# Kernel optimization log

Measured on AMD Instinct MI355X. Metric: run time of the kernel, lower is better.

Reference implementation:

```python
import jax, jax.numpy as jnp
import numpy as np

HIDDEN = 1024
NUM_HEADS = 16
HEAD_DIM = HIDDEN // NUM_HEADS
LN_EPS = 1e-12


def setup_inputs() -> dict:
    key = jax.random.key(0)
    ks = jax.random.split(key, 12)
    B, S, H = 4, 2048, HIDDEN
    scale = 0.02
    return {
        "hidden_states": jax.random.normal(ks[0], (B, S, H), dtype=jnp.float32),
        "attention_mask": jnp.zeros((B, 1, 1, S), dtype=jnp.float32),
        "Wq": jax.random.normal(ks[1], (H, H), dtype=jnp.float32) * scale,
        "bq": jnp.zeros((H,), dtype=jnp.float32),
        "Wk": jax.random.normal(ks[2], (H, H), dtype=jnp.float32) * scale,
        "bk": jnp.zeros((H,), dtype=jnp.float32),
        "Wv": jax.random.normal(ks[3], (H, H), dtype=jnp.float32) * scale,
        "bv": jnp.zeros((H,), dtype=jnp.float32),
        "Wo": jax.random.normal(ks[4], (H, H), dtype=jnp.float32) * scale,
        "bo": jnp.zeros((H,), dtype=jnp.float32),
        "ln_gamma": jnp.ones((H,), dtype=jnp.float32),
        "ln_beta": jnp.zeros((H,), dtype=jnp.float32),
    }


def _split_heads(x):  # [B,S,H] -> [B,nh,S,hd]
    B, S, _ = x.shape
    return x.reshape(B, S, NUM_HEADS, HEAD_DIM).transpose(0, 2, 1, 3)


def reference(hidden_states, attention_mask, Wq, bq, Wk, bk, Wv, bv, Wo, bo, ln_gamma, ln_beta):
    # QKV projections (torch Linear: x @ W.T + b)
    q = _split_heads(hidden_states @ Wq.T + bq)
    k = _split_heads(hidden_states @ Wk.T + bk)
    v = _split_heads(hidden_states @ Wv.T + bv)
    # scaled dot-product attention with additive mask (dropout=identity, eval)
    scores = jnp.einsum('bhqd,bhkd->bhqk', q, k) / jnp.sqrt(jnp.float32(HEAD_DIM))
    scores = scores + attention_mask
    probs = jax.nn.softmax(scores, axis=-1)
    ctx = jnp.einsum('bhqk,bhkd->bhqd', probs, v)
    B, _, S, _ = ctx.shape
    ctx = ctx.transpose(0, 2, 1, 3).reshape(B, S, HIDDEN)
    # output projection + residual + LayerNorm
    out = ctx @ Wo.T + bo + hidden_states
    mu = jnp.mean(out, axis=-1, keepdims=True)
    var = jnp.mean(jnp.square(out - mu), axis=-1, keepdims=True)
    return (out - mu) * jax.lax.rsqrt(var + LN_EPS) * ln_gamma + ln_beta
```

## Files before the change

### kernel.cpp

```cpp
#include <hip/hip_runtime.h>
#include <stdint.h>

#define SEQ   2048
#define BATCH 4
#define NH    16
#define HD    64
#define H     1024
#define QKVN  3072

typedef unsigned short u16;
typedef unsigned int   u32;
typedef __bf16 bf16x8 __attribute__((ext_vector_type(8)));
typedef float  f32x4  __attribute__((ext_vector_type(4)));
typedef unsigned int v2u  __attribute__((ext_vector_type(2)));
typedef unsigned int u32x4 __attribute__((ext_vector_type(4)));

#define MFMA16(a, b, c) __builtin_amdgcn_mfma_f32_16x16x32_bf16((a), (b), (c), 0, 0, 0)
#define LOG2E 1.4426950408889634f

__device__ __forceinline__ u16 f2bf(float f) {
  u32 u = __float_as_uint(f);
  u = (u + 0x7fffu + ((u >> 16) & 1u)) >> 16;
  return (u16)u;
}

__device__ __forceinline__ void gload16(const u16* g, u16* l) {
  __builtin_amdgcn_global_load_lds(
      (const __attribute__((address_space(1))) u32*)g,
      (__attribute__((address_space(3))) u32*)l, 16, 0, 0);
}

__device__ __forceinline__ u32 lds_addr(const void* p) {
  return (u32)(uintptr_t)(const __attribute__((address_space(3))) void*)p;
}

__global__ __launch_bounds__(256) void cast_all(
    const float* __restrict__ hid, const float* __restrict__ wq,
    const float* __restrict__ wk,  const float* __restrict__ wv,
    const float* __restrict__ wo,
    u16* __restrict__ hb, u16* __restrict__ wqkv, u16* __restrict__ wo_b)
{
  int i = blockIdx.x * 256 + threadIdx.x;
  const float* s; u16* d; int idx;
  if (i < 2097152) { s = hid; d = hb; idx = i; }
  else {
    int j = i - 2097152;
    int w = j >> 18; idx = j & 262143;
    if      (w == 0) { s = wq; d = wqkv; }
    else if (w == 1) { s = wk; d = wqkv + 1048576; }
    else if (w == 2) { s = wv; d = wqkv + 2097152; }
    else             { s = wo; d = wo_b; }
  }
  float4 v = ((const float4*)s)[idx];
  ushort4 o;
  o.x = f2bf(v.x); o.y = f2bf(v.y); o.z = f2bf(v.z); o.w = f2bf(v.w);
  ((ushort4*)d)[idx] = o;
}

template<int EPI>
__global__ __launch_bounds__(256, 2) void gemm_bf16(
    const u16* __restrict__ A, const u16* __restrict__ B,
    u16* __restrict__ outb, float* __restrict__ outf, int ldc,
    const float* __restrict__ b0, const float* __restrict__ b1,
    const float* __restrict__ b2, const float* __restrict__ resid)
{
  __shared__ __align__(16) u16 As[128 * 32];
  __shared__ __align__(16) u16 Bs[128 * 32];
  const int tid = threadIdx.x;
  const int lane = tid & 63;
  const int wv = tid >> 6, wr = wv >> 1, wc = wv & 1;
  const int l15 = lane & 15, l4 = lane >> 4;

  const int nwg = gridDim.x * gridDim.y;
  const int flat = blockIdx.y * gridDim.x + blockIdx.x;
  const int swz = (flat & 7) * (nwg >> 3) + (flat >> 3);
  const int row0 = (swz / gridDim.x) * 128, col0 = (swz % gridDim.x) * 128;

  const f32x4 fz = {0.f, 0.f, 0.f, 0.f};
  f32x4 acc[4][4];
#pragma unroll
  for (int i = 0; i < 4; ++i)
#pragma unroll
    for (int j = 0; j < 4; ++j) acc[i][j] = fz;

  const int srow = lane >> 2;
  const int skol = (lane & 3) * 8;
  const u16* Ab = A + (size_t)(row0 + srow) * 1024 + skol;
  const u16* Bb = B + (size_t)(col0 + srow) * 1024 + skol;
  const int c0 = wv * 2;

  for (int kt = 0; kt < 1024; kt += 32) {
    gload16(Ab + (size_t)(c0 * 16) * 1024 + kt,       &As[(c0 * 16) * 32]);
    gload16(Ab + (size_t)(c0 * 16 + 16) * 1024 + kt,  &As[(c0 * 16 + 16) * 32]);
    gload16(Bb + (size_t)(c0 * 16) * 1024 + kt,       &Bs[(c0 * 16) * 32]);
    gload16(Bb + (size_t)(c0 * 16 + 16) * 1024 + kt,  &Bs[(c0 * 16 + 16) * 32]);
    __syncthreads();

    bf16x8 af[4], bfr[4];
#pragma unroll
    for (int f = 0; f < 4; ++f) {
      af[f]  = *(const bf16x8*)&As[(wr * 64 + f * 16 + l15) * 32 + l4 * 8];
      bfr[f] = *(const bf16x8*)&Bs[(wc * 64 + f * 16 + l15) * 32 + l4 * 8];
    }
#pragma unroll
    for (int i = 0; i < 4; ++i)
#pragma unroll
      for (int j = 0; j < 4; ++j)
        acc[i][j] = MFMA16(af[i], bfr[j], acc[i][j]);
    __syncthreads();
  }

  if (EPI == 0) {
    const float* bias = (col0 < 1024) ? b0 : (col0 < 2048) ? b1 : b2;
#pragma unroll
    for (int i = 0; i < 4; ++i) {
      int gr0 = row0 + wr * 64 + i * 16 + l4 * 4;
#pragma unroll
      for (int j = 0; j < 4; ++j) {
        int gc = col0 + wc * 64 + j * 16 + l15;
        float bv = bias[gc & 1023];
#pragma unroll
        for (int r = 0; r < 4; ++r)
          outb[(size_t)(gr0 + r) * ldc + gc] = f2bf(acc[i][j][r] + bv);
      }
    }
  } else {
#pragma unroll
    for (int i = 0; i < 4; ++i) {
      int gr0 = row0 + wr * 64 + i * 16 + l4 * 4;
#pragma unroll
      for (int j = 0; j < 4; ++j) {
        int gc = col0 + wc * 64 + j * 16 + l15;
        float bv = b0[gc];
#pragma unroll
        for (int r = 0; r < 4; ++r) {
          size_t idx = (size_t)(gr0 + r) * ldc + gc;
          outf[idx] = acc[i][j][r] + bv + resid[idx];
        }
      }
    }
  }
}

__global__ __launch_bounds__(256, 2) void flash_attn(
    const u16* __restrict__ qkv, const float* __restrict__ mask,
    u16* __restrict__ ctxb)
{
  __shared__ __align__(16) u16 PQs[128 * 72];
  __shared__ __align__(16) u16 Ks[64 * 72];
  __shared__ __align__(16) u16 Vs[4096];

  const int flat = (blockIdx.z * 16 + blockIdx.y) * 16 + blockIdx.x;
  const int swzb = (flat & 7) * 128 + (flat >> 3);
  const int qt = swzb & 15, h = (swzb >> 4) & 15, b = swzb >> 8;

  const int tid = threadIdx.x, lane = tid & 63, wv = tid >> 6;
  const int l15 = lane & 15, l4 = lane >> 4;

  const size_t tokb = (size_t)b * SEQ;
  const u16* Qg = qkv + (tokb + (size_t)qt * 128) * QKVN + h * HD;
  const u16* Kg = qkv + tokb * QKVN + 1024 + h * HD;
  const u16* Vg = qkv + tokb * QKVN + 2048 + h * HD;
  const float* maskp = mask + (size_t)b * SEQ;

#pragma unroll
  for (int cc = 0; cc < 4; ++cc) {
    int c = tid + cc * 256;
    int r = c >> 3, ko = (c & 7) * 8;
    *(uint4*)&PQs[r * 72 + ko] = *(const uint4*)&Qg[(size_t)r * QKVN + ko];
  }
  __syncthreads();
  bf16x8 qf[2][2];
#pragma unroll
  for (int qfi = 0; qfi < 2; ++qfi)
#pragma unroll
    for (int ka = 0; ka < 2; ++ka)
      qf[qfi][ka] = *(const bf16x8*)&PQs[(wv * 32 + qfi * 16 + l15) * 72 + ka * 32 + l4 * 8];

  const f32x4 fz = {0.f, 0.f, 0.f, 0.f};
  float m_run[2][4], l_run[2][4];
  f32x4 ctx[2][4];
#pragma unroll
  for (int qfi = 0; qfi < 2; ++qfi)
#pragma unroll
    for (int r = 0; r < 4; ++r) { m_run[qfi][r] = -1e30f; l_run[qfi][r] = 0.f; }
#pragma unroll
  for (int qfi = 0; qfi < 2; ++qfi)
#pragma unroll
    for (int d = 0; d < 4; ++d) ctx[qfi][d] = fz;

  const int sr = tid >> 3, sk = (tid & 7) * 8;
  const int vso = (sk >> 4) * 1024 + (sk & 15);
  const u32 vaddr0 = lds_addr(&Vs[0]) + lane * 8 + (lane >> 4) * 128;

  uint4 kr0, kr1, vr0, vr1;
  kr0 = *(const uint4*)&Kg[(size_t)sr * QKVN + sk];
  kr1 = *(const uint4*)&Kg[(size_t)(sr + 32) * QKVN + sk];
  vr0 = *(const uint4*)&Vg[(size_t)sr * QKVN + sk];
  vr1 = *(const uint4*)&Vg[(size_t)(sr + 32) * QKVN + sk];

  for (int kv0 = 0; kv0 < SEQ; kv0 += 64) {
    *(uint4*)&Ks[sr * 72 + sk]        = kr0;
    *(uint4*)&Ks[(sr + 32) * 72 + sk] = kr1;
    *(uint4*)&Vs[vso + sr * 16]        = vr0;
    *(uint4*)&Vs[vso + (sr + 32) * 16] = vr1;
    __syncthreads();

    if (kv0 + 64 < SEQ) {
      kr0 = *(const uint4*)&Kg[(size_t)(kv0 + 64 + sr) * QKVN + sk];
      kr1 = *(const uint4*)&Kg[(size_t)(kv0 + 96 + sr) * QKVN + sk];
      vr0 = *(const uint4*)&Vg[(size_t)(kv0 + 64 + sr) * QKVN + sk];
      vr1 = *(const uint4*)&Vg[(size_t)(kv0 + 96 + sr) * QKVN + sk];
    }

    f32x4 s[2][4];
    __builtin_amdgcn_s_setprio(1);
#pragma unroll
    for (int nch = 0; nch < 4; ++nch) {
      bf16x8 kf0 = *(const bf16x8*)&Ks[(nch * 16 + l15) * 72 + l4 * 8];
      bf16x8 kf1 = *(const bf16x8*)&Ks[(nch * 16 + l15) * 72 + 32 + l4 * 8];
#pragma unroll
      for (int qfi = 0; qfi < 2; ++qfi) {
        f32x4 a = fz;
        a = MFMA16(qf[qfi][0], kf0, a);
        a = MFMA16(qf[qfi][1], kf1, a);
        s[qfi][nch] = a;
      }
    }
    __builtin_amdgcn_s_setprio(0);
    float mv[4];
#pragma unroll
    for (int nch = 0; nch < 4; ++nch) mv[nch] = maskp[kv0 + nch * 16 + l15] * LOG2E;
#pragma unroll
    for (int qfi = 0; qfi < 2; ++qfi)
#pragma unroll
      for (int nch = 0; nch < 4; ++nch)
#pragma unroll
        for (int r = 0; r < 4; ++r)
          s[qfi][nch][r] = s[qfi][nch][r] * (0.125f * LOG2E) + mv[nch];

#pragma unroll
    for (int qfi = 0; qfi < 2; ++qfi) {
      float mx[4], rs[4];
#pragma unroll
      for (int r = 0; r < 4; ++r)
        mx[r] = fmaxf(fmaxf(s[qfi][0][r], s[qfi][1][r]), fmaxf(s[qfi][2][r], s[qfi][3][r]));
#pragma unroll
      for (int d = 1; d < 16; d <<= 1)
#pragma unroll
        for (int r = 0; r < 4; ++r) mx[r] = fmaxf(mx[r], __shfl_xor(mx[r], d));
      bool need = false;
#pragma unroll
      for (int r = 0; r < 4; ++r) need |= (mx[r] > m_run[qfi][r] + 11.5415603f);
      if (__any((int)need)) {
#pragma unroll
        for (int r = 0; r < 4; ++r) {
          float mn = fmaxf(m_run[qfi][r], mx[r]);
          float al = exp2f(m_run[qfi][r] - mn);
          m_run[qfi][r] = mn;
          l_run[qfi][r] *= al;
#pragma unroll
          for (int d = 0; d < 4; ++d) ctx[qfi][d][r] *= al;
        }
      }
#pragma unroll
      for (int r = 0; r < 4; ++r) rs[r] = 0.f;
#pragma unroll
      for (int nch = 0; nch < 4; ++nch)
#pragma unroll
        for (int r = 0; r < 4; ++r) {
          float p = exp2f(s[qfi][nch][r] - m_run[qfi][r]);
          rs[r] += p;
          PQs[(wv * 32 + qfi * 16 + l4 * 4 + r) * 72 + nch * 16 + l15] = f2bf(p);
        }
#pragma unroll
      for (int d = 1; d < 16; d <<= 1)
#pragma unroll
        for (int r = 0; r < 4; ++r) rs[r] += __shfl_xor(rs[r], d);
#pragma unroll
      for (int r = 0; r < 4; ++r) l_run[qfi][r] += rs[r];
    }
    asm volatile("s_waitcnt lgkmcnt(0)" ::: "memory");

    bf16x8 pa[2][2];
#pragma unroll
    for (int qfi = 0; qfi < 2; ++qfi) {
      pa[qfi][0] = *(const bf16x8*)&PQs[(wv * 32 + qfi * 16 + l15) * 72 + l4 * 8];
      pa[qfi][1] = *(const bf16x8*)&PQs[(wv * 32 + qfi * 16 + l15) * 72 + 32 + l4 * 8];
    }
    __builtin_amdgcn_s_setprio(1);
#pragma unroll
    for (int d = 0; d < 4; ++d) {
      v2u t0, t1, t2, t3;
      u32 va = vaddr0 + d * 2048;
      asm volatile("ds_read_b64_tr_b16 %0, %1"             : "=&v"(t0) : "v"(va));
      asm volatile("ds_read_b64_tr_b16 %0, %1 offset:128"  : "=&v"(t1) : "v"(va));
      asm volatile("ds_read_b64_tr_b16 %0, %1 offset:1024" : "=&v"(t2) : "v"(va));
      asm volatile("ds_read_b64_tr_b16 %0, %1 offset:1152" : "=&v"(t3) : "v"(va));
      asm volatile("s_waitcnt lgkmcnt(0)");
      __builtin_amdgcn_sched_barrier(0);
      u32x4 w0 = {t0[0], t0[1], t1[0], t1[1]};
      u32x4 w1 = {t2[0], t2[1], t3[0], t3[1]};
      bf16x8 vf0 = __builtin_bit_cast(bf16x8, w0);
      bf16x8 vf1 = __builtin_bit_cast(bf16x8, w1);
      ctx[0][d] = MFMA16(pa[0][0], vf0, ctx[0][d]);
      ctx[0][d] = MFMA16(pa[0][1], vf1, ctx[0][d]);
      ctx[1][d] = MFMA16(pa[1][0], vf0, ctx[1][d]);
      ctx[1][d] = MFMA16(pa[1][1], vf1, ctx[1][d]);
    }
    __builtin_amdgcn_s_setprio(0);
    __syncthreads();
  }

#pragma unroll
  for (int qfi = 0; qfi < 2; ++qfi)
#pragma unroll
    for (int d = 0; d < 4; ++d)
#pragma unroll
      for (int r = 0; r < 4; ++r) {
        int gr = qt * 128 + wv * 32 + qfi * 16 + l4 * 4 + r;
        float o = ctx[qfi][d][r] / l_run[qfi][r];
        ctxb[(tokb + gr) * (size_t)H + h * HD + d * 16 + l15] = f2bf(o);
      }
}

__global__ __launch_bounds__(256) void ln_res(const float* __restrict__ x,
    const float* __restrict__ gamma, const float* __restrict__ beta,
    float* __restrict__ out)
{
  const int row = blockIdx.x, t = threadIdx.x;
  float4 v = ((const float4*)(x + (size_t)row * H))[t];
  float s1 = v.x + v.y + v.z + v.w;
  float s2 = v.x * v.x + v.y * v.y + v.z * v.z + v.w * v.w;
#pragma unroll
  for (int d = 1; d < 64; d <<= 1) { s1 += __shfl_xor(s1, d); s2 += __shfl_xor(s2, d); }
  __shared__ float a1[4], a2[4];
  if ((t & 63) == 0) { a1[t >> 6] = s1; a2[t >> 6] = s2; }
  __syncthreads();
  s1 = a1[0] + a1[1] + a1[2] + a1[3];
  s2 = a2[0] + a2[1] + a2[2] + a2[3];
  float mu  = s1 * (1.f / H);
  float var = s2 * (1.f / H) - mu * mu;
  float rstd = rsqrtf(var + 1e-12f);
  float4 g  = ((const float4*)gamma)[t];
  float4 be = ((const float4*)beta)[t];
  float4 o;
  o.x = (v.x - mu) * rstd * g.x + be.x;
  o.y = (v.y - mu) * rstd * g.y + be.y;
  o.z = (v.z - mu) * rstd * g.z + be.z;
  o.w = (v.w - mu) * rstd * g.w + be.w;
  ((float4*)(out + (size_t)row * H))[t] = o;
}

extern "C" void kernel_launch(void* const* d_in, const int* in_sizes, int n_in,
                              void* d_out, int out_size, void* d_ws, size_t ws_size,
                              hipStream_t stream)
{
  const float* hid  = (const float*)d_in[0];
  const float* mask = (const float*)d_in[1];
  const float* Wq   = (const float*)d_in[2];
  const float* bq   = (const float*)d_in[3];
  const float* Wk   = (const float*)d_in[4];
  const float* bk   = (const float*)d_in[5];
  const float* Wv   = (const float*)d_in[6];
  const float* bv   = (const float*)d_in[7];
  const float* Wo   = (const float*)d_in[8];
  const float* bo   = (const float*)d_in[9];
  const float* gam  = (const float*)d_in[10];
  const float* bet  = (const float*)d_in[11];

  char* ws = (char*)d_ws;
  u16*   hb   = (u16*)(ws);
  u16*   wqkv = (u16*)(ws + 16777216);
  u16*   wo_b = (u16*)(ws + 23068672);
  u16*   qkvb = (u16*)(ws + 25165824);
  u16*   ctxb = (u16*)(ws + 75497472);
  float* tmp  = (float*)(ws + 25165824);

  cast_all<<<12288, 256, 0, stream>>>(hid, Wq, Wk, Wv, Wo, hb, wqkv, wo_b);

  gemm_bf16<0><<<dim3(24, 64), 256, 0, stream>>>(hb, wqkv, qkvb, nullptr, QKVN,
                                                 bq, bk, bv, nullptr);
  flash_attn<<<dim3(16, NH, BATCH), 256, 0, stream>>>(qkvb, mask, ctxb);
  gemm_bf16<1><<<dim3(8, 64), 256, 0, stream>>>(ctxb, wo_b, nullptr, tmp, H,
                                                bo, nullptr, nullptr, hid);
  ln_res<<<8192, 256, 0, stream>>>(tmp, gam, bet, (float*)d_out);
}
```

Before: 434.4 us.

## Rewrite flash attention with 32x32 MFMA, swizzled LDS and register-resident P

Switches the attention kernel from 16x16x32 to 32x32x16 bf16 MFMA and computes S transposed (K as A operand), so each lane owns a single query's softmax state. P is packed to bf16 with v_cvt_pk and rearranged with permlane32_swap instead of going through LDS, which removes the P store/reload and a wait. Q/K tiles use XOR-swizzled unpadded LDS instead of padded rows. The cost is more register pressure from the 16-wide accumulators, extra shuffles for rescaling and normalization, and a more complex V layout.

```diff
diff --git a/kernel.cpp b/kernel.cpp
--- a/kernel.cpp
+++ b/kernel.cpp
@@ -12,11 +12,14 @@
 typedef unsigned int   u32;
 typedef __bf16 bf16x8 __attribute__((ext_vector_type(8)));
 typedef float  f32x4  __attribute__((ext_vector_type(4)));
-typedef unsigned int v2u  __attribute__((ext_vector_type(2)));
+typedef float  f32x16 __attribute__((ext_vector_type(16)));
+typedef unsigned int v2u   __attribute__((ext_vector_type(2)));
 typedef unsigned int u32x4 __attribute__((ext_vector_type(4)));
 
 #define MFMA16(a, b, c) __builtin_amdgcn_mfma_f32_16x16x32_bf16((a), (b), (c), 0, 0, 0)
+#define MFMA32(a, b, c) __builtin_amdgcn_mfma_f32_32x32x16_bf16((a), (b), (c), 0, 0, 0)
 #define LOG2E 1.4426950408889634f
+#define SC    (0.125f * LOG2E)
 
 __device__ __forceinline__ u16 f2bf(float f) {
   u32 u = __float_as_uint(f);
@@ -32,6 +35,12 @@
 
 __device__ __forceinline__ u32 lds_addr(const void* p) {
   return (u32)(uintptr_t)(const __attribute__((address_space(3))) void*)p;
+}
+
+__device__ __forceinline__ u32 cvtpk(float lo, float hi) {
+  u32 r;
+  asm("v_cvt_pk_bf16_f32 %0, %1, %2" : "=v"(r) : "v"(lo), "v"(hi));
+  return r;
 }
 
 __global__ __launch_bounds__(256) void cast_all(
@@ -146,16 +155,16 @@
     const u16* __restrict__ qkv, const float* __restrict__ mask,
     u16* __restrict__ ctxb)
 {
-  __shared__ __align__(16) u16 PQs[128 * 72];
-  __shared__ __align__(16) u16 Ks[64 * 72];
+  __shared__ __align__(16) u16 Qs[128 * 64];
+  __shared__ __align__(16) u16 Ks[64 * 64];
   __shared__ __align__(16) u16 Vs[4096];
 
   const int flat = (blockIdx.z * 16 + blockIdx.y) * 16 + blockIdx.x;
   const int swzb = (flat & 7) * 128 + (flat >> 3);
   const int qt = swzb & 15, h = (swzb >> 4) & 15, b = swzb >> 8;
 
-  const int tid = threadIdx.x, lane = tid & 63, wv = tid >> 6;
-  const int l15 = lane & 15, l4 = lane >> 4;
+  const int tid = threadIdx.x, lane = tid & 63, wq = tid >> 6;
+  const int l31 = lane & 31, l15 = lane & 15, h5 = lane >> 5;
 
   const size_t tokb = (size_t)b * SEQ;
   const u16* Qg = qkv + (tokb + (size_t)qt * 128) * QKVN + h * HD;
@@ -167,43 +176,43 @@
   for (int cc = 0; cc < 4; ++cc) {
     int c = tid + cc * 256;
     int r = c >> 3, ko = (c & 7) * 8;
-    *(uint4*)&PQs[r * 72 + ko] = *(const uint4*)&Qg[(size_t)r * QKVN + ko];
+    u32 qb = (u32)(r * 128 + ko * 2) ^ ((r & 7) << 4);
+    *(uint4*)((char*)Qs + qb) = *(const uint4*)&Qg[(size_t)r * QKVN + ko];
   }
   __syncthreads();
-  bf16x8 qf[2][2];
-#pragma unroll
-  for (int qfi = 0; qfi < 2; ++qfi)
-#pragma unroll
-    for (int ka = 0; ka < 2; ++ka)
-      qf[qfi][ka] = *(const bf16x8*)&PQs[(wv * 32 + qfi * 16 + l15) * 72 + ka * 32 + l4 * 8];
-
-  const f32x4 fz = {0.f, 0.f, 0.f, 0.f};
-  float m_run[2][4], l_run[2][4];
-  f32x4 ctx[2][4];
-#pragma unroll
-  for (int qfi = 0; qfi < 2; ++qfi)
-#pragma unroll
-    for (int r = 0; r < 4; ++r) { m_run[qfi][r] = -1e30f; l_run[qfi][r] = 0.f; }
-#pragma unroll
-  for (int qfi = 0; qfi < 2; ++qfi)
-#pragma unroll
-    for (int d = 0; d < 4; ++d) ctx[qfi][d] = fz;
+
+  const u32 swzl = (u32)((l31 & 7) << 4);
+  u32 cb[4];
+#pragma unroll
+  for (int kb = 0; kb < 4; ++kb)
+    cb[kb] = ((u32)(kb * 32 + h5 * 16)) ^ swzl;
+
+  bf16x8 qf[4];
+#pragma unroll
+  for (int kb = 0; kb < 4; ++kb)
+    qf[kb] = *(const bf16x8*)((char*)Qs + (u32)((wq * 32 + l31) * 128) + cb[kb]);
+
+  float m_run = -1e30f, l_run = 0.f;
+  f32x16 ctx0 = {}, ctx1 = {};
 
   const int sr = tid >> 3, sk = (tid & 7) * 8;
-  const int vso = (sk >> 4) * 1024 + (sk & 15);
-  const u32 vaddr0 = lds_addr(&Vs[0]) + lane * 8 + (lane >> 4) * 128;
-
-  uint4 kr0, kr1, vr0, vr1;
-  kr0 = *(const uint4*)&Kg[(size_t)sr * QKVN + sk];
-  kr1 = *(const uint4*)&Kg[(size_t)(sr + 32) * QKVN + sk];
-  vr0 = *(const uint4*)&Vg[(size_t)sr * QKVN + sk];
-  vr1 = *(const uint4*)&Vg[(size_t)(sr + 32) * QKVN + sk];
+  const u32 kwb0 = ((u32)(sr * 128 + sk * 2)) ^ ((sr & 7) << 4);
+  const u32 kwb1 = ((u32)((sr + 32) * 128 + sk * 2)) ^ ((sr & 7) << 4);
+  const u32 vw0 = (u32)((sk >> 4) * 1024 + (sr >> 2) * 64 + (sr & 3) * 16 + (sk & 15));
+  const u32 vw1 = (u32)((sk >> 4) * 1024 + ((sr + 32) >> 2) * 64 + (sr & 3) * 16 + (sk & 15));
+
+  const u32 vaddr = lds_addr(Vs) + (u32)(l15 * 8 + ((lane >> 4) & 1) * 2048 + h5 * 256);
+
+  uint4 kr0 = *(const uint4*)&Kg[(size_t)sr * QKVN + sk];
+  uint4 kr1 = *(const uint4*)&Kg[(size_t)(sr + 32) * QKVN + sk];
+  uint4 vr0 = *(const uint4*)&Vg[(size_t)sr * QKVN + sk];
+  uint4 vr1 = *(const uint4*)&Vg[(size_t)(sr + 32) * QKVN + sk];
 
   for (int kv0 = 0; kv0 < SEQ; kv0 += 64) {
-    *(uint4*)&Ks[sr * 72 + sk]        = kr0;
-    *(uint4*)&Ks[(sr + 32) * 72 + sk] = kr1;
-    *(uint4*)&Vs[vso + sr * 16]        = vr0;
-    *(uint4*)&Vs[vso + (sr + 32) * 16] = vr1;
+    *(uint4*)((char*)Ks + kwb0) = kr0;
+    *(uint4*)((char*)Ks + kwb1) = kr1;
+    *(uint4*)&Vs[vw0] = vr0;
+    *(uint4*)&Vs[vw1] = vr1;
     __syncthreads();
 
     if (kv0 + 64 < SEQ) {
@@ -213,115 +222,111 @@
       vr1 = *(const uint4*)&Vg[(size_t)(kv0 + 96 + sr) * QKVN + sk];
     }
 
-    f32x4 s[2][4];
+    f32x16 s0 = {}, s1 = {};
     __builtin_amdgcn_s_setprio(1);
 #pragma unroll
-    for (int nch = 0; nch < 4; ++nch) {
-      bf16x8 kf0 = *(const bf16x8*)&Ks[(nch * 16 + l15) * 72 + l4 * 8];
-      bf16x8 kf1 = *(const bf16x8*)&Ks[(nch * 16 + l15) * 72 + 32 + l4 * 8];
-#pragma unroll
-      for (int qfi = 0; qfi < 2; ++qfi) {
-        f32x4 a = fz;
-        a = MFMA16(qf[qfi][0], kf0, a);
-        a = MFMA16(qf[qfi][1], kf1, a);
-        s[qfi][nch] = a;
-      }
+    for (int kb = 0; kb < 4; ++kb) {
+      bf16x8 a0 = *(const bf16x8*)((char*)Ks + (u32)(l31 * 128) + cb[kb]);
+      bf16x8 a1 = *(const bf16x8*)((char*)Ks + (u32)(l31 * 128 + 4096) + cb[kb]);
+      s0 = MFMA32(a0, qf[kb], s0);
+      s1 = MFMA32(a1, qf[kb], s1);
     }
     __builtin_amdgcn_s_setprio(0);
-    float mv[4];
-#pragma unroll
-    for (int nch = 0; nch < 4; ++nch) mv[nch] = maskp[kv0 + nch * 16 + l15] * LOG2E;
-#pragma unroll
-    for (int qfi = 0; qfi < 2; ++qfi)
-#pragma unroll
-      for (int nch = 0; nch < 4; ++nch)
-#pragma unroll
-        for (int r = 0; r < 4; ++r)
-          s[qfi][nch][r] = s[qfi][nch][r] * (0.125f * LOG2E) + mv[nch];
-
-#pragma unroll
-    for (int qfi = 0; qfi < 2; ++qfi) {
-      float mx[4], rs[4];
-#pragma unroll
-      for (int r = 0; r < 4; ++r)
-        mx[r] = fmaxf(fmaxf(s[qfi][0][r], s[qfi][1][r]), fmaxf(s[qfi][2][r], s[qfi][3][r]));
-#pragma unroll
-      for (int d = 1; d < 16; d <<= 1)
-#pragma unroll
-        for (int r = 0; r < 4; ++r) mx[r] = fmaxf(mx[r], __shfl_xor(mx[r], d));
-      bool need = false;
-#pragma unroll
-      for (int r = 0; r < 4; ++r) need |= (mx[r] > m_run[qfi][r] + 11.5415603f);
-      if (__any((int)need)) {
-#pragma unroll
-        for (int r = 0; r < 4; ++r) {
-          float mn = fmaxf(m_run[qfi][r], mx[r]);
-          float al = exp2f(m_run[qfi][r] - mn);
-          m_run[qfi][r] = mn;
-          l_run[qfi][r] *= al;
-#pragma unroll
-          for (int d = 0; d < 4; ++d) ctx[qfi][d][r] *= al;
-        }
-      }
-#pragma unroll
-      for (int r = 0; r < 4; ++r) rs[r] = 0.f;
-#pragma unroll
-      for (int nch = 0; nch < 4; ++nch)
-#pragma unroll
-        for (int r = 0; r < 4; ++r) {
-          float p = exp2f(s[qfi][nch][r] - m_run[qfi][r]);
-          rs[r] += p;
-          PQs[(wv * 32 + qfi * 16 + l4 * 4 + r) * 72 + nch * 16 + l15] = f2bf(p);
-        }
-#pragma unroll
-      for (int d = 1; d < 16; d <<= 1)
-#pragma unroll
-        for (int r = 0; r < 4; ++r) rs[r] += __shfl_xor(rs[r], d);
-#pragma unroll
-      for (int r = 0; r < 4; ++r) l_run[qfi][r] += rs[r];
-    }
-    asm volatile("s_waitcnt lgkmcnt(0)" ::: "memory");
-
-    bf16x8 pa[2][2];
-#pragma unroll
-    for (int qfi = 0; qfi < 2; ++qfi) {
-      pa[qfi][0] = *(const bf16x8*)&PQs[(wv * 32 + qfi * 16 + l15) * 72 + l4 * 8];
-      pa[qfi][1] = *(const bf16x8*)&PQs[(wv * 32 + qfi * 16 + l15) * 72 + 32 + l4 * 8];
-    }
+
+#pragma unroll
+    for (int r = 0; r < 16; ++r) {
+      int kvr = kv0 + (r & 3) + 8 * (r >> 2);
+      float ma = maskp[kvr],      mb = maskp[kvr + 4];
+      float mc = maskp[kvr + 32], md = maskp[kvr + 36];
+      float mv0 = (h5 ? mb : ma) * LOG2E;
+      float mv1 = (h5 ? md : mc) * LOG2E;
+      s0[r] = s0[r] * SC + mv0;
+      s1[r] = s1[r] * SC + mv1;
+    }
+
+    float mx = s0[0];
+#pragma unroll
+    for (int r = 1; r < 16; ++r) mx = fmaxf(mx, s0[r]);
+#pragma unroll
+    for (int r = 0; r < 16; ++r) mx = fmaxf(mx, s1[r]);
+    mx = fmaxf(mx, __shfl_xor(mx, 32));
+
+    bool need = (mx > m_run + 11.5415603f);
+    if (__any((int)need)) {
+      float mn = fmaxf(m_run, mx);
+      float al = exp2f(m_run - mn);
+      m_run = mn;
+      l_run *= al;
+#pragma unroll
+      for (int r = 0; r < 16; ++r) {
+        float av = __shfl(al, (r & 3) + 8 * (r >> 2) + 4 * h5);
+        ctx0[r] *= av;
+        ctx1[r] *= av;
+      }
+    }
+
+    float ps = 0.f;
+#pragma unroll
+    for (int r = 0; r < 16; ++r) { s0[r] = exp2f(s0[r] - m_run); ps += s0[r]; }
+#pragma unroll
+    for (int r = 0; r < 16; ++r) { s1[r] = exp2f(s1[r] - m_run); ps += s1[r]; }
+    ps += __shfl_xor(ps, 32);
+    l_run += ps;
+
+    bf16x8 paf[4];
+#pragma unroll
+    for (int blk = 0; blk < 4; ++blk) {
+      u32 w0, w1, w2, w3;
+      if (blk < 2) {
+        int r0 = blk * 8;
+        w0 = cvtpk(s0[r0 + 0], s0[r0 + 1]); w1 = cvtpk(s0[r0 + 2], s0[r0 + 3]);
+        w2 = cvtpk(s0[r0 + 4], s0[r0 + 5]); w3 = cvtpk(s0[r0 + 6], s0[r0 + 7]);
+      } else {
+        int r0 = (blk - 2) * 8;
+        w0 = cvtpk(s1[r0 + 0], s1[r0 + 1]); w1 = cvtpk(s1[r0 + 2], s1[r0 + 3]);
+        w2 = cvtpk(s1[r0 + 4], s1[r0 + 5]); w3 = cvtpk(s1[r0 + 6], s1[r0 + 7]);
+      }
+      asm volatile("v_permlane32_swap_b32 %0, %1" : "+v"(w0), "+v"(w2));
+      asm volatile("v_permlane32_swap_b32 %0, %1" : "+v"(w1), "+v"(w3));
+      u32x4 ww = {w0, w1, w2, w3};
+      paf[blk] = __builtin_bit_cast(bf16x8, ww);
+    }
+
     __builtin_amdgcn_s_setprio(1);
 #pragma unroll
-    for (int d = 0; d < 4; ++d) {
-      v2u t0, t1, t2, t3;
-      u32 va = vaddr0 + d * 2048;
-      asm volatile("ds_read_b64_tr_b16 %0, %1"             : "=&v"(t0) : "v"(va));
-      asm volatile("ds_read_b64_tr_b16 %0, %1 offset:128"  : "=&v"(t1) : "v"(va));
-      asm volatile("ds_read_b64_tr_b16 %0, %1 offset:1024" : "=&v"(t2) : "v"(va));
-      asm volatile("ds_read_b64_tr_b16 %0, %1 offset:1152" : "=&v"(t3) : "v"(va));
+    for (int db = 0; db < 2; ++db) {
+      v2u t[8];
+#pragma unroll
+      for (int kb = 0; kb < 4; ++kb) {
+        asm volatile("ds_read_b64_tr_b16 %0, %1 offset:%c2"
+                     : "=&v"(t[kb * 2])     : "v"(vaddr), "i"(db * 4096 + kb * 512));
+        asm volatile("ds_read_b64_tr_b16 %0, %1 offset:%c2"
+                     : "=&v"(t[kb * 2 + 1]) : "v"(vaddr), "i"(db * 4096 + kb * 512 + 128));
+      }
       asm volatile("s_waitcnt lgkmcnt(0)");
       __builtin_amdgcn_sched_barrier(0);
-      u32x4 w0 = {t0[0], t0[1], t1[0], t1[1]};
-      u32x4 w1 = {t2[0], t2[1], t3[0], t3[1]};
-      bf16x8 vf0 = __builtin_bit_cast(bf16x8, w0);
-      bf16x8 vf1 = __builtin_bit_cast(bf16x8, w1);
-      ctx[0][d] = MFMA16(pa[0][0], vf0, ctx[0][d]);
-      ctx[0][d] = MFMA16(pa[0][1], vf1, ctx[0][d]);
-      ctx[1][d] = MFMA16(pa[1][0], vf0, ctx[1][d]);
-      ctx[1][d] = MFMA16(pa[1][1], vf1, ctx[1][d]);
+#pragma unroll
+      for (int kb = 0; kb < 4; ++kb) {
+        u32x4 ww = {t[kb * 2][0], t[kb * 2][1], t[kb * 2 + 1][0], t[kb * 2 + 1][1]};
+        bf16x8 vf = __builtin_bit_cast(bf16x8, ww);
+        if (db == 0) ctx0 = MFMA32(paf[kb], vf, ctx0);
+        else         ctx1 = MFMA32(paf[kb], vf, ctx1);
+      }
     }
     __builtin_amdgcn_s_setprio(0);
     __syncthreads();
   }
 
-#pragma unroll
-  for (int qfi = 0; qfi < 2; ++qfi)
-#pragma unroll
-    for (int d = 0; d < 4; ++d)
-#pragma unroll
-      for (int r = 0; r < 4; ++r) {
-        int gr = qt * 128 + wv * 32 + qfi * 16 + l4 * 4 + r;
-        float o = ctx[qfi][d][r] / l_run[qfi][r];
-        ctxb[(tokb + gr) * (size_t)H + h * HD + d * 16 + l15] = f2bf(o);
-      }
+  float linv = 1.0f / l_run;
+#pragma unroll
+  for (int r = 0; r < 16; ++r) {
+    int qidx = (r & 3) + 8 * (r >> 2) + 4 * h5;
+    float li = __shfl(linv, qidx);
+    int gr = qt * 128 + wq * 32 + qidx;
+    u16* o = &ctxb[(tokb + gr) * (size_t)H + h * HD + l31];
+    o[0]  = f2bf(ctx0[r] * li);
+    o[32] = f2bf(ctx1[r] * li);
+  }
 }
 
 __global__ __launch_bounds__(256) void ln_res(const float* __restrict__ x,
```

Result: faster. 361.7 us (-16.7%).
